# Performance work log

Measured on AMD Instinct MI355X. Metric: run time of the kernel, lower is better.

The kernel has to match this reference:

```python
import jax, jax.numpy as jnp
import numpy as np

MUL = 128            # channel multiplicity (node feature channels)
Z = 10               # number of chemical elements (node_attrs dim)
L_DIMS = (1, 3, 5, 7)   # edge SH irrep dims, lmax=3
MM_DIMS = (1, 3)        # magmom SH irrep dims, lmax=1
AVG_NUM_NEIGHBORS = 20.0
N_NODES = 5000
N_EDGES = 100000
R_DIM = 8            # edge radial feature dim
MM_INV_DIM = 8       # magmom invariant feature dim


def _mlp(x, Ws, act):
    # e3nn FullyConnectedNet: variance-preserving linear layers, act between hidden layers
    for W in Ws[:-1]:
        h = x @ W * (1.0 / np.sqrt(W.shape[0]))
        x = act(h) if act is not None else h
    return x @ Ws[-1] * (1.0 / np.sqrt(Ws[-1].shape[0]))


def _conv_tp(x, sh, w, dims):
    # channelwise 'uvu' tensor product: (MUL x 0e) x SH(l) -> MUL x l per l.
    # x:[E,MUL], sh:[E,sum(dims)], w:[E,MUL,n_l]. CG for 0e x l -> l is trivial.
    outs, off = [], 0
    for l, d in enumerate(dims):
        blk = (w[:, :, l] * x)[:, :, None] * sh[:, None, off:off + d]  # [E,MUL,d]
        outs.append(blk.reshape(x.shape[0], MUL * d))
        off += d
    return jnp.concatenate(outs, axis=-1)


def _per_l_linear(x, Ws, dims):
    # e3nn o3.Linear: per-l channel mixing with 1/sqrt(fan_in) normalization
    outs, off = [], 0
    scale = 1.0 / np.sqrt(MUL)
    for l, d in enumerate(dims):
        blk = x[:, off:off + MUL * d].reshape(-1, MUL, d)
        outs.append((jnp.einsum('nud,uv->nvd', blk, Ws[l]) * scale).reshape(-1, MUL * d))
        off += MUL * d
    return jnp.concatenate(outs, axis=-1)


def _skip_tp(x, attrs, Ws, dims):
    # FullyConnectedTensorProduct(irreps_out, Zx0e, irreps_out): per-l bilinear mix
    outs, off = [], 0
    scale = 1.0 / np.sqrt(MUL * attrs.shape[-1])
    for l, d in enumerate(dims):
        blk = x[:, off:off + MUL * d].reshape(-1, MUL, d)
        outs.append((jnp.einsum('nud,nz,uzv->nvd', blk, attrs, Ws[l]) * scale).reshape(-1, MUL * d))
        off += MUL * d
    return jnp.concatenate(outs, axis=-1)


def _reshape_irreps(x, dims):
    # [N, sum(MUL*d)] -> [N, MUL, sum(d)]
    outs, off = [], 0
    for d in dims:
        outs.append(x[:, off:off + MUL * d].reshape(-1, MUL, d))
        off += MUL * d
    return jnp.concatenate(outs, axis=-1)


def setup_inputs() -> dict:
    key = jax.random.key(0)
    ks = jax.random.split(key, 24)
    E, N = N_EDGES, N_NODES
    inp = {
        'node_attrs': jax.random.uniform(ks[0], (N, Z), jnp.float32),
        'node_feats': jax.random.normal(ks[1], (N, MUL), jnp.float32),
        'edge_attrs': jax.random.normal(ks[2], (E, sum(L_DIMS)), jnp.float32),
        'edge_feats': jax.random.uniform(ks[3], (E, R_DIM), jnp.float32),
        'magmom_node_inv_feats': jax.random.normal(ks[4], (N, MM_INV_DIM), jnp.float32),
        'magmom_node_attrs': jax.random.normal(ks[5], (N, sum(MM_DIMS)), jnp.float32),
        'edge_index': jax.random.randint(ks[6], (2, E), 0, N),
    }
    rin = R_DIM + MM_INV_DIM
    inp['W_up'] = jax.random.normal(ks[7], (MUL, MUL), jnp.float32)
    inp['W_rad1'] = jax.random.normal(ks[8], (rin, 64), jnp.float32)
    inp['W_rad2'] = jax.random.normal(ks[9], (64, 64), jnp.float32)
    inp['W_rad3'] = jax.random.normal(ks[10], (64, 64), jnp.float32)
    inp['W_rad4'] = jax.random.normal(ks[11], (64, MUL * len(L_DIMS)), jnp.float32)  # weight_numel=512
    inp['M_rad1'] = jax.random.normal(ks[12], (rin, 64), jnp.float32)
    inp['M_rad2'] = jax.random.normal(ks[13], (64, 64), jnp.float32)
    inp['M_rad3'] = jax.random.normal(ks[14], (64, 64), jnp.float32)
    inp['M_rad4'] = jax.random.normal(ks[15], (64, MUL * len(MM_DIMS)), jnp.float32)  # weight_numel=256
    inp['W_density'] = jax.random.normal(ks[16], (R_DIM, 1), jnp.float32)
    inp['W_lin'] = jax.random.normal(ks[17], (len(L_DIMS), MUL, MUL), jnp.float32)
    inp['W_mlin'] = jax.random.normal(ks[18], (len(MM_DIMS), MUL, MUL), jnp.float32)
    inp['W_skip'] = jax.random.normal(ks[19], (len(L_DIMS), MUL, Z, MUL), jnp.float32)
    inp['W_mskip'] = jax.random.normal(ks[20], (len(L_DIMS), MUL, Z, MUL), jnp.float32)
    return inp


def reference(node_attrs, node_feats, edge_attrs, edge_feats, magmom_node_inv_feats,
              magmom_node_attrs, W_up, W_rad1, W_rad2, W_rad3, W_rad4,
              M_rad1, M_rad2, M_rad3, M_rad4, W_density, W_lin, W_mlin,
              W_skip, W_mskip, edge_index):
    sender, receiver = edge_index[0], edge_index[1]
    E = edge_attrs.shape[0]
    N = node_feats.shape[0]
    silu = jax.nn.silu

    x = node_feats @ W_up * (1.0 / np.sqrt(MUL))  # linear_up
    xj = x[sender]                                # [E, MUL]
    ef_mm = jnp.concatenate([edge_feats, magmom_node_inv_feats[sender]], axis=-1)  # [E, 16]

    tp_w = _mlp(ef_mm, [W_rad1, W_rad2, W_rad3, W_rad4], silu)          # [E, 512]
    edge_density = jnp.tanh((edge_feats @ W_density * (1.0 / np.sqrt(R_DIM))) ** 2)  # [E, 1]

    w4 = tp_w.reshape(E, MUL, len(L_DIMS))
    pre_mji = _conv_tp(xj, edge_attrs, w4, L_DIMS)                      # [E, 2048]

    w_mm = _mlp(ef_mm, [M_rad1, M_rad2, M_rad3, M_rad4], None).reshape(E, MUL, len(MM_DIMS))
    w_mm = w_mm * pre_mji[:, :MUL][:, :, None]                          # density-gated by scalar part
    magmom_mji = _conv_tp(xj, magmom_node_attrs[sender], w_mm, MM_DIMS) # [E, 512]

    w4b = w4 * magmom_mji[:, :MUL][:, :, None]
    mji = _conv_tp(xj, edge_attrs, w4b, L_DIMS)                         # [E, 2048]

    density = jax.ops.segment_sum(edge_density, receiver, num_segments=N)  # [N, 1]
    msg = jax.ops.segment_sum(mji, receiver, num_segments=N)               # [N, 2048]
    mm_msg = jax.ops.segment_sum(magmom_mji, receiver, num_segments=N)     # [N, 512]

    msg = _per_l_linear(msg, W_lin, L_DIMS) / (density + 1.0)
    msg = _skip_tp(msg, node_attrs, W_skip, L_DIMS)

    mm = _per_l_linear(mm_msg, W_mlin, MM_DIMS) / AVG_NUM_NEIGHBORS
    # magmom_linear maps (128x0e+128x1o) -> target irreps: l=2,3 outputs have no path -> zero
    mm = jnp.concatenate([mm, jnp.zeros((N, MUL * (5 + 7)), mm.dtype)], axis=-1)
    mm = _skip_tp(mm, node_attrs, W_mskip, L_DIMS)

    out1 = _reshape_irreps(msg, L_DIMS)  # [N, 128, 16]
    out2 = _reshape_irreps(mm, L_DIMS)   # [N, 128, 16]
    return jnp.stack([out1, out2], axis=0)
```

## Files before the change

kernel.cpp:

```cpp
#include <hip/hip_runtime.h>
#include <hip/hip_fp16.h>
#include <stdint.h>


__device__ __forceinline__ float silu_f(float x) {
  return x / (1.0f + __expf(-x));
}

union F2H2 { float f; __half2 h; };

__global__ void k_zero_int(int* p, int n) {
  int i = blockIdx.x * blockDim.x + threadIdx.x;
  if (i < n) p[i] = 0;
}

__global__ __launch_bounds__(256) void k_prep(
    const float* __restrict__ M1, const float* __restrict__ M2,
    const float* __restrict__ M3, const float* __restrict__ M4,
    float* __restrict__ Mc) {
  __shared__ float T1[16 * 64];
  __shared__ float T2[16 * 64];
  int t = threadIdx.x;
  for (int i = t; i < 16 * 64; i += 256) {
    int r = i >> 6, c = i & 63;
    float s = 0.f;
    for (int k = 0; k < 64; k++) s += M1[r * 64 + k] * M2[k * 64 + c];
    T1[i] = s;
  }
  __syncthreads();
  for (int i = t; i < 16 * 64; i += 256) {
    int r = i >> 6, c = i & 63;
    float s = 0.f;
    for (int k = 0; k < 64; k++) s += T1[r * 64 + k] * M3[k * 64 + c];
    T2[i] = s;
  }
  __syncthreads();
  for (int i = t; i < 16 * 256; i += 256) {
    int r = i >> 8, c = i & 255;
    float s = 0.f;
    for (int k = 0; k < 64; k++) s += T2[r * 64 + k] * M4[k * 256 + c];
    Mc[i] = s * (1.0f / 2048.0f);
  }
}

__global__ __launch_bounds__(256) void k_w4h(const float* __restrict__ W4,
                                             __half2* __restrict__ W4h) {
  int k = blockIdx.x;
  int t = threadIdx.x;
  W4h[k * 256 + t] =
      __halves2half2(__float2half(W4[k * 512 + t]), __float2half(W4[k * 512 + t + 256]));
}

__global__ __launch_bounds__(128) void k_up(const float* __restrict__ nf,
                                            const float* __restrict__ W,
                                            float* __restrict__ x, int Nn) {
  int n = blockIdx.x;
  int v = threadIdx.x;
  __shared__ float row[128];
  row[v] = nf[n * 128 + v];
  __syncthreads();
  float s = 0.f;
#pragma unroll 8
  for (int k = 0; k < 128; k++) s += row[k] * W[k * 128 + v];
  x[n * 128 + v] = s * 0.08838834764831845f;
}

__global__ void k_count(const int* __restrict__ recv, int* __restrict__ deg, int E) {
  int e = blockIdx.x * blockDim.x + threadIdx.x;
  if (e < E) atomicAdd(&deg[recv[e]], 1);
}

__global__ __launch_bounds__(1024) void k_scan(const int* __restrict__ deg,
                                               int* __restrict__ rowstart,
                                               int* __restrict__ cursor, int Nn) {
  __shared__ int part[1024];
  int t = threadIdx.x;
  int chunk = (Nn + 1023) / 1024;
  int lo = t * chunk;
  int hi = lo + chunk; if (hi > Nn) hi = Nn; if (lo > Nn) lo = Nn;
  int s = 0;
  for (int i = lo; i < hi; i++) s += deg[i];
  part[t] = s;
  __syncthreads();
  for (int o = 1; o < 1024; o <<= 1) {
    int v = (t >= o) ? part[t - o] : 0;
    __syncthreads();
    part[t] += v;
    __syncthreads();
  }
  int base = (t == 0) ? 0 : part[t - 1];
  for (int i = lo; i < hi; i++) {
    rowstart[i] = base;
    cursor[i] = base;
    base += deg[i];
  }
  if (t == 1023) rowstart[Nn] = part[1023];
}

__global__ void k_fill(const int* __restrict__ recv, int* __restrict__ cursor,
                       int* __restrict__ elist, int E) {
  int e = blockIdx.x * blockDim.x + threadIdx.x;
  if (e < E) {
    int p = atomicAdd(&cursor[recv[e]], 1);
    elist[p] = e;
  }
}

__global__ __launch_bounds__(256) void k_edge_hA(
    const float* __restrict__ edge_feats, const float* __restrict__ mminv,
    const int* __restrict__ sender,
    const float* __restrict__ W1, const float* __restrict__ W2,
    const float* __restrict__ W3, const float* __restrict__ Wd,
    float* __restrict__ hAe, float* __restrict__ dens, int E) {
  const int base = blockIdx.x * 8;
  const int t = threadIdx.x;
  __shared__ float ef[8][16];
  __shared__ float hA[8][64];
  __shared__ float hB[8][64];
  const int gwave = t >> 6;
  const int o6 = t & 63;

  if (t < 128) {
    int g = t >> 4, j = t & 15;
    int e = base + g;
    float v = 0.f;
    if (e < E) v = (j < 8) ? edge_feats[e * 8 + j] : mminv[sender[e] * 8 + (j - 8)];
    ef[g][j] = v;
  } else if (t < 136) {
    int g = t - 128;
    int e = base + g;
    if (e < E) {
      float q = 0.f;
#pragma unroll
      for (int k = 0; k < 8; k++) q += edge_feats[e * 8 + k] * Wd[k];
      q *= 0.35355339059327373f;
      dens[e] = tanhf(q * q);
    }
  }
  __syncthreads();

#pragma unroll
  for (int rep = 0; rep < 2; rep++) {
    int g = gwave + rep * 4;
    float s = 0.f;
#pragma unroll
    for (int k = 0; k < 16; k++) s += ef[g][k] * W1[k * 64 + o6];
    hA[g][o6] = silu_f(s * 0.25f);
  }
#pragma unroll
  for (int rep = 0; rep < 2; rep++) {
    int g = gwave + rep * 4;
    float s = 0.f;
#pragma unroll 8
    for (int k = 0; k < 64; k++) s += hA[g][k] * W2[k * 64 + o6];
    hB[g][o6] = silu_f(s * 0.125f);
  }
#pragma unroll
  for (int rep = 0; rep < 2; rep++) {
    int g = gwave + rep * 4;
    float s = 0.f;
#pragma unroll 8
    for (int k = 0; k < 64; k++) s += hB[g][k] * W3[k * 64 + o6];
    int e = base + g;
    if (e < E) hAe[(size_t)e * 64 + o6] = silu_f(s * 0.125f);
  }
}

__global__ __launch_bounds__(256) void k_gather_raw(
    const float* __restrict__ x, const float* __restrict__ edge_attrs,
    const float* __restrict__ edge_feats, const float* __restrict__ mminv,
    const float* __restrict__ mmattrs, const int* __restrict__ sender,
    const __half2* __restrict__ W4h, const float* __restrict__ Mc,
    const float* __restrict__ dens, const float* __restrict__ hAe,
    const int* __restrict__ rowstart, const int* __restrict__ elist,
    float* __restrict__ msg, float* __restrict__ mmr, float* __restrict__ densN,
    int Nn) {
  const int n = blockIdx.x;
  const int t = threadIdx.x;
  const int start = rowstart[n], end = rowstart[n + 1];

  __shared__ float ef[8][16];
  __shared__ float hA[8][64];
  __shared__ float ubuf[8 * 512 + 8 * 256];
  __shared__ float xjs[8][128];
  __shared__ float shs[8][16];
  __shared__ float mmshs[8][4];
  __shared__ float denss[8];
  __shared__ int eS[8], sS[8];

  float (*w4s)[512] = (float (*)[512])ubuf;
  float (*wmms)[256] = (float (*)[256])(ubuf + 8 * 512);

  float accm[8] = {0, 0, 0, 0, 0, 0, 0, 0};
  float accmm0 = 0.f, accmm1 = 0.f;
  float accd = 0.f;

  const int u = t & 127;
  const int half = t >> 7;

  for (int base = start; base < end; base += 8) {
    if (t < 8) {
      int g = t;
      if (base + g < end) {
        int e = elist[base + g];
        eS[g] = e;
        sS[g] = sender[e];
        denss[g] = dens[e];
      } else {
        eS[g] = -1;
        sS[g] = 0;
        denss[g] = 0.f;
      }
    }
    __syncthreads();
    if (t < 128) {
      int g = t >> 4, j = t & 15;
      int e = eS[g];
      shs[g][j] = (e >= 0) ? edge_attrs[e * 16 + j] : 0.f;
      float v = 0.f;
      if (e >= 0) v = (j < 8) ? edge_feats[e * 8 + j] : mminv[sS[g] * 8 + (j - 8)];
      ef[g][j] = v;
    } else if (t < 160) {
      int g = (t - 128) >> 2, j = (t - 128) & 3;
      mmshs[g][j] = (eS[g] >= 0) ? mmattrs[sS[g] * 4 + j] : 0.f;
    }
    for (int i = t; i < 1024; i += 256) {
      int g = i >> 7, uu = i & 127;
      xjs[g][uu] = (eS[g] >= 0) ? x[(size_t)sS[g] * 128 + uu] : 0.f;
    }
    for (int i = t; i < 512; i += 256) {
      int g = i >> 6, k = i & 63;
      hA[g][k] = (eS[g] >= 0) ? hAe[(size_t)eS[g] * 64 + k] : 0.f;
    }
    __syncthreads();

    {
      float a[8] = {0, 0, 0, 0, 0, 0, 0, 0};
      float b[8] = {0, 0, 0, 0, 0, 0, 0, 0};
#pragma unroll 8
      for (int k = 0; k < 64; k++) {
        __half2 w2 = W4h[k * 256 + t];
        float w0 = __low2float(w2);
        float w1 = __high2float(w2);
#pragma unroll
        for (int g = 0; g < 8; g++) {
          float h = hA[g][k];
          a[g] += h * w0;
          b[g] += h * w1;
        }
      }
      int p0 = (t & 3) * 128 + (t >> 2);
      int p1 = (t & 3) * 128 + 64 + (t >> 2);
#pragma unroll
      for (int g = 0; g < 8; g++) {
        w4s[g][p0] = a[g] * 0.125f;
        w4s[g][p1] = b[g] * 0.125f;
      }
    }
    {
      float c[8] = {0, 0, 0, 0, 0, 0, 0, 0};
#pragma unroll
      for (int k = 0; k < 16; k++) {
        float w = Mc[k * 256 + t];
#pragma unroll
        for (int g = 0; g < 8; g++) c[g] += ef[g][k] * w;
      }
      int p = (t & 1) * 128 + (t >> 1);
#pragma unroll
      for (int g = 0; g < 8; g++) wmms[g][p] = c[g];
    }
    __syncthreads();

#pragma unroll 2
    for (int g = 0; g < 8; g++) {
      float w40 = w4s[g][u];
      float w41 = w4s[g][128 + u];
      float w42 = w4s[g][256 + u];
      float w43 = w4s[g][384 + u];
      float wm0 = wmms[g][u];
      float wm1 = wmms[g][128 + u];
      float xj = xjs[g][u];
      float sh0 = shs[g][0];
      float pre0 = w40 * xj * sh0;
      float wg0 = wm0 * pre0;
      float wg1 = wm1 * pre0;
      float mm0 = wg0 * xj * mmshs[g][0];
      float m1 = wg1 * xj;
      float bx = mm0 * xj;
      float b0 = w40 * bx, b1 = w41 * bx, b2 = w42 * bx, b3 = w43 * bx;
      if (half == 0) {
        accmm0 += mm0;
        accmm1 += m1 * mmshs[g][1];
        accm[0] += b0 * sh0;
        accm[1] += b1 * shs[g][1];
        accm[2] += b1 * shs[g][2];
        accm[3] += b1 * shs[g][3];
        accm[4] += b2 * shs[g][4];
        accm[5] += b2 * shs[g][5];
        accm[6] += b2 * shs[g][6];
        accm[7] += b2 * shs[g][7];
      } else {
        accmm0 += m1 * mmshs[g][2];
        accmm1 += m1 * mmshs[g][3];
        accm[0] += b2 * shs[g][8];
        accm[1] += b3 * shs[g][9];
        accm[2] += b3 * shs[g][10];
        accm[3] += b3 * shs[g][11];
        accm[4] += b3 * shs[g][12];
        accm[5] += b3 * shs[g][13];
        accm[6] += b3 * shs[g][14];
        accm[7] += b3 * shs[g][15];
      }
    }
    if (t == 0) {
#pragma unroll
      for (int g = 0; g < 8; g++) accd += denss[g];
    }
  }

  float4* mp = (float4*)(msg + (size_t)n * 2048 + u * 16 + half * 8);
  mp[0] = make_float4(accm[0], accm[1], accm[2], accm[3]);
  mp[1] = make_float4(accm[4], accm[5], accm[6], accm[7]);
  *(float2*)(mmr + (size_t)n * 512 + u * 4 + half * 2) = make_float2(accmm0, accmm1);
  if (t == 0) densN[n] = accd;
}

__global__ void k_zero2(float* __restrict__ out2, int Nn) {
  int i = blockIdx.x * blockDim.x + threadIdx.x;
  if (i < Nn * 128) {
    float4 z = make_float4(0.f, 0.f, 0.f, 0.f);
    float4* p = (float4*)(out2 + (size_t)i * 16);
    p[1] = z;
    p[2] = z;
    p[3] = z;
  }
}

__global__ __launch_bounds__(128) void k_wt(const float* __restrict__ Wskip,
                                            const float* __restrict__ Wmskip,
                                            __half* __restrict__ Wt) {
  int bx = blockIdx.x;
  int L = bx >> 7, u = bx & 127;
  int v = threadIdx.x;
  const float* src = (L < 4) ? (Wskip + (size_t)L * 163840)
                             : (Wmskip + (size_t)(L - 4) * 163840);
  __half* dst = Wt + (((size_t)L * 128 + u) * 128 + v) * 12;
#pragma unroll
  for (int z = 0; z < 10; z++) dst[z] = __float2half(src[u * 1280 + z * 128 + v]);
  dst[10] = __float2half(0.f);
  dst[11] = __float2half(0.f);
}

template <int D, int SP>
__device__ __forceinline__ void skip2_body(
    const float* __restrict__ attrs, const float* __restrict__ in, int in_rs,
    int in_us, int in_cb, const float* __restrict__ Wl,
    const float* __restrict__ densN, float basescl, bool useDinv,
    const __half* __restrict__ Wt, float* __restrict__ outp, int out_cb,
    int Nn, int n0, float* lin_s, float (*attrs_s)[10]) {
  const int t = threadIdx.x;
  for (int i = t; i < 80; i += 256) {
    int nn = i / 10, z = i - nn * 10;
    int n = n0 + nn;
    attrs_s[nn][z] = (n < Nn) ? attrs[n * 10 + z] : 0.f;
  }
  for (int i = t; i < 8 * 128 * D; i += 256) {
    int nn = i / (128 * D);
    int r = i - nn * 128 * D;
    int uu = r / D;
    int m = r - uu * D;
    int n = n0 + nn;
    lin_s[(nn * 128 + uu) * SP + m] =
        (n < Nn) ? in[(size_t)n * in_rs + uu * in_us + in_cb + m] : 0.f;
  }
  __syncthreads();

  const int v = t & 127, hf = t >> 7;

  float lm[4][D];
#pragma unroll
  for (int q = 0; q < 4; q++)
#pragma unroll
    for (int m = 0; m < D; m++) lm[q][m] = 0.f;
  for (int uu = 0; uu < 128; uu++) {
    float wv = Wl[uu * 128 + v];
#pragma unroll
    for (int q = 0; q < 4; q++) {
      const float* ls = &lin_s[((hf * 4 + q) * 128 + uu) * SP];
#pragma unroll
      for (int m = 0; m < D; m++) lm[q][m] += ls[m] * wv;
    }
  }
  __syncthreads();
#pragma unroll
  for (int q = 0; q < 4; q++) {
    int nd = n0 + hf * 4 + q;
    float scl = basescl;
    if (useDinv) scl *= 1.0f / (((nd < Nn) ? densN[nd] : 0.f) + 1.0f);
    float* ls = &lin_s[((hf * 4 + q) * 128 + v) * SP];
#pragma unroll
    for (int m = 0; m < D; m++) ls[m] = lm[q][m] * scl;
  }
  __syncthreads();

  float ar[4][10];
#pragma unroll
  for (int q = 0; q < 4; q++)
#pragma unroll
    for (int z = 0; z < 10; z++) ar[q][z] = attrs_s[hf * 4 + q][z];

  float acc[4][D];
#pragma unroll
  for (int q = 0; q < 4; q++)
#pragma unroll
    for (int m = 0; m < D; m++) acc[q][m] = 0.f;

  const __half* wp0 = Wt + (size_t)v * 12;
  for (int u = 0; u < 128; u++) {
    const __half* wp = wp0 + (size_t)u * 1536;
    const float2* fp = (const float2*)wp;
    float2 q0 = fp[0];
    float2 q1 = fp[1];
    float2 q2 = fp[2];
    F2H2 c0, c1, c2, c3, c4;
    c0.f = q0.x; c1.f = q0.y; c2.f = q1.x; c3.f = q1.y; c4.f = q2.x;
    float wr[10];
    wr[0] = __low2float(c0.h); wr[1] = __high2float(c0.h);
    wr[2] = __low2float(c1.h); wr[3] = __high2float(c1.h);
    wr[4] = __low2float(c2.h); wr[5] = __high2float(c2.h);
    wr[6] = __low2float(c3.h); wr[7] = __high2float(c3.h);
    wr[8] = __low2float(c4.h); wr[9] = __high2float(c4.h);
#pragma unroll
    for (int q = 0; q < 4; q++) {
      float wn = 0.f;
#pragma unroll
      for (int z = 0; z < 10; z++) wn += ar[q][z] * wr[z];
      const float* ls = &lin_s[((hf * 4 + q) * 128 + u) * SP];
#pragma unroll
      for (int m = 0; m < D; m++) acc[q][m] += ls[m] * wn;
    }
  }
#pragma unroll
  for (int q = 0; q < 4; q++) {
    int n = n0 + hf * 4 + q;
    if (n < Nn) {
      float* op = outp + (size_t)n * 2048 + v * 16 + out_cb;
#pragma unroll
      for (int m = 0; m < D; m++) op[m] = acc[q][m] * 0.027950849718747371f;
    }
  }
}

__global__ __launch_bounds__(256) void k_skip2(
    const float* __restrict__ attrs, const float* __restrict__ msg,
    const float* __restrict__ mmr, const float* __restrict__ densN,
    const float* __restrict__ Wlin, const float* __restrict__ Wmlin,
    const __half* __restrict__ Wt, float* __restrict__ out, int Nn) {
  __shared__ float lin_s[8 * 128 * 8];
  __shared__ float attrs_s[8][10];
  const int n0 = blockIdx.x * 8;
  const int job = blockIdx.y;
  const __half* Wtj = Wt + (size_t)job * 128 * 128 * 12;
  const float scl = 0.08838834764831845f;
  const float sm = 0.08838834764831845f / 20.0f;
  switch (job) {
    case 0: skip2_body<1, 1>(attrs, msg, 2048, 16, 0, Wlin, densN, scl, true, Wtj, out, 0, Nn, n0, lin_s, attrs_s); break;
    case 1: skip2_body<3, 4>(attrs, msg, 2048, 16, 1, Wlin + 16384, densN, scl, true, Wtj, out, 1, Nn, n0, lin_s, attrs_s); break;
    case 2: skip2_body<5, 8>(attrs, msg, 2048, 16, 4, Wlin + 32768, densN, scl, true, Wtj, out, 4, Nn, n0, lin_s, attrs_s); break;
    case 3: skip2_body<7, 8>(attrs, msg, 2048, 16, 9, Wlin + 49152, densN, scl, true, Wtj, out, 9, Nn, n0, lin_s, attrs_s); break;
    case 4: skip2_body<1, 1>(attrs, mmr, 512, 4, 0, Wmlin, densN, sm, false, Wtj, out + (size_t)Nn * 2048, 0, Nn, n0, lin_s, attrs_s); break;
    case 5: skip2_body<3, 4>(attrs, mmr, 512, 4, 1, Wmlin + 16384, densN, sm, false, Wtj, out + (size_t)Nn * 2048, 1, Nn, n0, lin_s, attrs_s); break;
  }
}

__global__ __launch_bounds__(256) void k_gather_f(
    const float* __restrict__ x, const float* __restrict__ edge_attrs,
    const float* __restrict__ edge_feats, const float* __restrict__ mminv,
    const float* __restrict__ mmattrs, const int* __restrict__ sender,
    const float* __restrict__ W1, const float* __restrict__ W2,
    const float* __restrict__ W3, const float* __restrict__ W4,
    const float* __restrict__ Mc, const float* __restrict__ Wd,
    const float* __restrict__ Wlin, const float* __restrict__ Wmlin,
    const int* __restrict__ rowstart, const int* __restrict__ elist,
    float* __restrict__ linm, float* __restrict__ linmm, int Nn) {
  const int n = blockIdx.x;
  const int t = threadIdx.x;
  const int start = rowstart[n], end = rowstart[n + 1];

  __shared__ float ef[8][16];
  __shared__ float hA[8][64];
  __shared__ float hB[8][64];
  __shared__ float ubuf[8 * 512 + 8 * 256];
  __shared__ float xjs[8][128];
  __shared__ float shs[8][16];
  __shared__ float mmshs[8][4];
  __shared__ float denss[8];
  __shared__ int eS[8], sS[8];
  __shared__ float dsum_s;

  float (*w4s)[512] = (float (*)[512])ubuf;
  float (*wmms)[256] = (float (*)[256])(ubuf + 8 * 512);
  float (*msg_s)[17] = (float (*)[17])ubuf;
  float (*mm_s)[5] = (float (*)[5])(ubuf + 128 * 17);

  float accm[8] = {0, 0, 0, 0, 0, 0, 0, 0};
  float accmm0 = 0.f, accmm1 = 0.f;
  float accd = 0.f;

  const int u = t & 127;
  const int half = t >> 7;
  const int gwave = t >> 6;
  const int o6 = t & 63;

  for (int base = start; base < end; base += 8) {
    if (t < 8) {
      int g = t;
      if (base + g < end) {
        int e = elist[base + g];
        eS[g] = e;
        sS[g] = sender[e];
      } else {
        eS[g] = -1;
        sS[g] = 0;
        denss[g] = 0.f;
      }
    }
    __syncthreads();
    if (t < 128) {
      int g = t >> 4, j = t & 15;
      int e = eS[g];
      shs[g][j] = (e >= 0) ? edge_attrs[e * 16 + j] : 0.f;
      float v = 0.f;
      if (e >= 0) v = (j < 8) ? edge_feats[e * 8 + j] : mminv[sS[g] * 8 + (j - 8)];
      ef[g][j] = v;
    } else if (t < 160) {
      int g = (t - 128) >> 2, j = (t - 128) & 3;
      mmshs[g][j] = (eS[g] >= 0) ? mmattrs[sS[g] * 4 + j] : 0.f;
    }
    for (int i = t; i < 1024; i += 256) {
      int g = i >> 7, uu = i & 127;
      xjs[g][uu] = (eS[g] >= 0) ? x[(size_t)sS[g] * 128 + uu] : 0.f;
    }
    if (t < 8 && eS[t] >= 0) {
      int e = eS[t];
      float q = 0.f;
#pragma unroll
      for (int k = 0; k < 8; k++) q += edge_feats[e * 8 + k] * Wd[k];
      q *= 0.35355339059327373f;
      denss[t] = tanhf(q * q);
    }
    __syncthreads();

#pragma unroll
    for (int rep = 0; rep < 2; rep++) {
      int g = gwave + rep * 4;
      float s = 0.f;
#pragma unroll
      for (int k = 0; k < 16; k++) s += ef[g][k] * W1[k * 64 + o6];
      hA[g][o6] = silu_f(s * 0.25f);
    }
#pragma unroll
    for (int rep = 0; rep < 2; rep++) {
      int g = gwave + rep * 4;
      float s = 0.f;
#pragma unroll 8
      for (int k = 0; k < 64; k++) s += hA[g][k] * W2[k * 64 + o6];
      hB[g][o6] = silu_f(s * 0.125f);
    }
#pragma unroll
    for (int rep = 0; rep < 2; rep++) {
      int g = gwave + rep * 4;
      float s = 0.f;
#pragma unroll 8
      for (int k = 0; k < 64; k++) s += hB[g][k] * W3[k * 64 + o6];
      hA[g][o6] = silu_f(s * 0.125f);
    }
    __syncthreads();
    {
      float a[8] = {0, 0, 0, 0, 0, 0, 0, 0};
      float b[8] = {0, 0, 0, 0, 0, 0, 0, 0};
#pragma unroll 8
      for (int k = 0; k < 64; k++) {
        float w0 = W4[k * 512 + t];
        float w1 = W4[k * 512 + t + 256];
#pragma unroll
        for (int g = 0; g < 8; g++) {
          float h = hA[g][k];
          a[g] += h * w0;
          b[g] += h * w1;
        }
      }
      int p0 = (t & 3) * 128 + (t >> 2);
      int p1 = (t & 3) * 128 + 64 + (t >> 2);
#pragma unroll
      for (int g = 0; g < 8; g++) {
        w4s[g][p0] = a[g] * 0.125f;
        w4s[g][p1] = b[g] * 0.125f;
      }
    }
    {
      float c[8] = {0, 0, 0, 0, 0, 0, 0, 0};
#pragma unroll
      for (int k = 0; k < 16; k++) {
        float w = Mc[k * 256 + t];
#pragma unroll
        for (int g = 0; g < 8; g++) c[g] += ef[g][k] * w;
      }
      int p = (t & 1) * 128 + (t >> 1);
#pragma unroll
      for (int g = 0; g < 8; g++) wmms[g][p] = c[g];
    }
    __syncthreads();
#pragma unroll 2
    for (int g = 0; g < 8; g++) {
      float xj = xjs[g][u];
      float sh0 = shs[g][0];
      float w40 = w4s[g][u];
      float w41 = w4s[g][128 + u];
      float w42 = w4s[g][256 + u];
      float w43 = w4s[g][384 + u];
      float pre0 = w40 * xj * sh0;
      float wg0 = wmms[g][u] * pre0;
      float wg1 = wmms[g][128 + u] * pre0;
      float mm0 = wg0 * xj * mmshs[g][0];
      float m1 = wg1 * xj;
      float bx = mm0 * xj;
      float b0 = w40 * bx, b1 = w41 * bx, b2 = w42 * bx, b3 = w43 * bx;
      if (half == 0) {
        accmm0 += mm0;
        accmm1 += m1 * mmshs[g][1];
        accm[0] += b0 * sh0;
        accm[1] += b1 * shs[g][1];
        accm[2] += b1 * shs[g][2];
        accm[3] += b1 * shs[g][3];
        accm[4] += b2 * shs[g][4];
        accm[5] += b2 * shs[g][5];
        accm[6] += b2 * shs[g][6];
        accm[7] += b2 * shs[g][7];
      } else {
        accmm0 += m1 * mmshs[g][2];
        accmm1 += m1 * mmshs[g][3];
        accm[0] += b2 * shs[g][8];
        accm[1] += b3 * shs[g][9];
        accm[2] += b3 * shs[g][10];
        accm[3] += b3 * shs[g][11];
        accm[4] += b3 * shs[g][12];
        accm[5] += b3 * shs[g][13];
        accm[6] += b3 * shs[g][14];
        accm[7] += b3 * shs[g][15];
      }
    }
    if (t == 0) {
#pragma unroll
      for (int g = 0; g < 8; g++) accd += denss[g];
    }
  }

  __syncthreads();
#pragma unroll
  for (int j = 0; j < 8; j++) msg_s[u][half * 8 + j] = accm[j];
  mm_s[u][half * 2 + 0] = accmm0;
  mm_s[u][half * 2 + 1] = accmm1;
  if (t == 0) dsum_s = accd;
  __syncthreads();
  const float dinv = 1.0f / (dsum_s + 1.0f);

  float outl[8] = {0, 0, 0, 0, 0, 0, 0, 0};
  if (half == 0) {
    for (int uu = 0; uu < 128; uu++) {
      float wl0 = Wlin[uu * 128 + u];
      float wl1 = Wlin[16384 + uu * 128 + u];
      float wl2 = Wlin[32768 + uu * 128 + u];
      outl[0] += msg_s[uu][0] * wl0;
      outl[1] += msg_s[uu][1] * wl1;
      outl[2] += msg_s[uu][2] * wl1;
      outl[3] += msg_s[uu][3] * wl1;
      outl[4] += msg_s[uu][4] * wl2;
      outl[5] += msg_s[uu][5] * wl2;
      outl[6] += msg_s[uu][6] * wl2;
      outl[7] += msg_s[uu][7] * wl2;
    }
  } else {
    for (int uu = 0; uu < 128; uu++) {
      float wl2 = Wlin[32768 + uu * 128 + u];
      float wl3 = Wlin[49152 + uu * 128 + u];
      outl[0] += msg_s[uu][8] * wl2;
      outl[1] += msg_s[uu][9] * wl3;
      outl[2] += msg_s[uu][10] * wl3;
      outl[3] += msg_s[uu][11] * wl3;
      outl[4] += msg_s[uu][12] * wl3;
      outl[5] += msg_s[uu][13] * wl3;
      outl[6] += msg_s[uu][14] * wl3;
      outl[7] += msg_s[uu][15] * wl3;
    }
  }
  const float sclv = 0.08838834764831845f * dinv;
  float4 v0 = make_float4(outl[0] * sclv, outl[1] * sclv, outl[2] * sclv, outl[3] * sclv);
  float4 v1 = make_float4(outl[4] * sclv, outl[5] * sclv, outl[6] * sclv, outl[7] * sclv);
  float4* lp = (float4*)(linm + (size_t)n * 2048 + u * 16 + half * 8);
  lp[0] = v0;
  lp[1] = v1;

  float om0 = 0.f, om1 = 0.f;
  if (half == 0) {
    for (int uu = 0; uu < 128; uu++) {
      om0 += mm_s[uu][0] * Wmlin[uu * 128 + u];
      om1 += mm_s[uu][1] * Wmlin[16384 + uu * 128 + u];
    }
  } else {
    for (int uu = 0; uu < 128; uu++) {
      float wm1 = Wmlin[16384 + uu * 128 + u];
      om0 += mm_s[uu][2] * wm1;
      om1 += mm_s[uu][3] * wm1;
    }
  }
  const float sm = 0.08838834764831845f / 20.0f;
  *(float2*)(linmm + (size_t)n * 512 + u * 4 + half * 2) = make_float2(om0 * sm, om1 * sm);
}

template <int D, int SP>
__device__ __forceinline__ void skip_body2(
    const float* __restrict__ attrs, const float* __restrict__ in, int in_rs,
    int in_us, int in_cb, const __half* __restrict__ Wt, float* __restrict__ outp,
    int out_cb, int Nn, int n0, float* lin_s, float (*attrs_s)[10]) {
  const int t = threadIdx.x;
  for (int i = t; i < 160; i += 256) {
    int nn = i / 10, z = i - nn * 10;
    int n = n0 + nn;
    attrs_s[nn][z] = (n < Nn) ? attrs[n * 10 + z] : 0.f;
  }
  for (int i = t; i < 16 * 128 * D; i += 256) {
    int nn = i / (128 * D);
    int r = i - nn * 128 * D;
    int uu = r / D;
    int m = r - uu * D;
    int n = n0 + nn;
    lin_s[(nn * 128 + uu) * SP + m] =
        (n < Nn) ? in[(size_t)n * in_rs + uu * in_us + in_cb + m] : 0.f;
  }
  __syncthreads();

  const int v = t & 127, hf = t >> 7;
  float ar[8][10];
#pragma unroll
  for (int q = 0; q < 8; q++)
#pragma unroll
    for (int z = 0; z < 10; z++) ar[q][z] = attrs_s[hf * 8 + q][z];

  float acc[8][D];
#pragma unroll
  for (int q = 0; q < 8; q++)
#pragma unroll
    for (int m = 0; m < D; m++) acc[q][m] = 0.f;

  const __half* wp0 = Wt + (size_t)v * 12;
  for (int u = 0; u < 128; u++) {
    const __half* wp = wp0 + (size_t)u * 1536;
    const float2* fp = (const float2*)wp;
    float2 q0 = fp[0];
    float2 q1 = fp[1];
    float2 q2 = fp[2];
    F2H2 c0, c1, c2, c3, c4;
    c0.f = q0.x; c1.f = q0.y; c2.f = q1.x; c3.f = q1.y; c4.f = q2.x;
    float wr[10];
    wr[0] = __low2float(c0.h); wr[1] = __high2float(c0.h);
    wr[2] = __low2float(c1.h); wr[3] = __high2float(c1.h);
    wr[4] = __low2float(c2.h); wr[5] = __high2float(c2.h);
    wr[6] = __low2float(c3.h); wr[7] = __high2float(c3.h);
    wr[8] = __low2float(c4.h); wr[9] = __high2float(c4.h);
#pragma unroll
    for (int q = 0; q < 8; q++) {
      float wn = 0.f;
#pragma unroll
      for (int z = 0; z < 10; z++) wn += ar[q][z] * wr[z];
      const float* ls = &lin_s[((hf * 8 + q) * 128 + u) * SP];
#pragma unroll
      for (int m = 0; m < D; m++) acc[q][m] += ls[m] * wn;
    }
  }
#pragma unroll
  for (int q = 0; q < 8; q++) {
    int n = n0 + hf * 8 + q;
    if (n < Nn) {
      float* op = outp + (size_t)n * 2048 + v * 16 + out_cb;
#pragma unroll
      for (int m = 0; m < D; m++) op[m] = acc[q][m] * 0.027950849718747371f;
    }
  }
}

__global__ __launch_bounds__(256) void k_skip(
    const float* __restrict__ attrs, const float* __restrict__ linm,
    const float* __restrict__ linmm, const __half* __restrict__ Wt,
    float* __restrict__ out, int Nn) {
  __shared__ float lin_s[16 * 128 * 8];
  __shared__ float attrs_s[16][10];
  const int n0 = blockIdx.x * 16;
  const int job = blockIdx.y;
  const __half* Wtj = Wt + (size_t)job * 128 * 128 * 12;
  switch (job) {
    case 0: skip_body2<1, 1>(attrs, linm, 2048, 16, 0, Wtj, out, 0, Nn, n0, lin_s, attrs_s); break;
    case 1: skip_body2<3, 4>(attrs, linm, 2048, 16, 1, Wtj, out, 1, Nn, n0, lin_s, attrs_s); break;
    case 2: skip_body2<5, 8>(attrs, linm, 2048, 16, 4, Wtj, out, 4, Nn, n0, lin_s, attrs_s); break;
    case 3: skip_body2<7, 8>(attrs, linm, 2048, 16, 9, Wtj, out, 9, Nn, n0, lin_s, attrs_s); break;
    case 4: skip_body2<1, 1>(attrs, linmm, 512, 4, 0, Wtj, out + (size_t)Nn * 2048, 0, Nn, n0, lin_s, attrs_s); break;
    case 5: skip_body2<3, 4>(attrs, linmm, 512, 4, 1, Wtj, out + (size_t)Nn * 2048, 1, Nn, n0, lin_s, attrs_s); break;
  }
}

extern "C" void kernel_launch(void* const* d_in, const int* in_sizes, int n_in,
                              void* d_out, int out_size, void* d_ws, size_t ws_size,
                              hipStream_t stream) {
  const float* node_attrs = (const float*)d_in[0];
  const float* node_feats = (const float*)d_in[1];
  const float* edge_attrs = (const float*)d_in[2];
  const float* edge_feats = (const float*)d_in[3];
  const float* mminv = (const float*)d_in[4];
  const float* mmattrs = (const float*)d_in[5];
  const int* edge_index = (const int*)d_in[6];
  const float* W_up = (const float*)d_in[7];
  const float* W1 = (const float*)d_in[8];
  const float* W2 = (const float*)d_in[9];
  const float* W3 = (const float*)d_in[10];
  const float* W4 = (const float*)d_in[11];
  const float* M1 = (const float*)d_in[12];
  const float* M2 = (const float*)d_in[13];
  const float* M3 = (const float*)d_in[14];
  const float* M4 = (const float*)d_in[15];
  const float* Wd = (const float*)d_in[16];
  const float* Wlin = (const float*)d_in[17];
  const float* Wmlin = (const float*)d_in[18];
  const float* Wskip = (const float*)d_in[19];
  const float* Wmskip = (const float*)d_in[20];

  const int N = in_sizes[1] / 128;
  const int E = in_sizes[2] / 16;
  const int* sender = edge_index;
  const int* recv = edge_index + E;

  float* ws = (float*)d_ws;
  float* x = ws;     ws += (size_t)N * 128;
  float* Mc = ws;    ws += 16 * 256;
  __half* Wt = (__half*)ws;  ws += (size_t)6 * 128 * 128 * 12 / 2;
  __half2* W4h = (__half2*)ws; ws += 64 * 256;
  float* msg = ws;   ws += (size_t)N * 2048;
  float* mmr = ws;   ws += (size_t)N * 512;
  float* densN = ws; ws += N;
  float* dens = ws;  ws += E;
  int* ibuf = (int*)ws;
  int* rowstart = ibuf;
  int* deg = ibuf + (N + 1);
  int* cursor = deg + N;
  int* elist = cursor + N;
  float* hAe = (float*)(((uintptr_t)(elist + E) + 63) & ~(uintptr_t)63);
  size_t need = (size_t)((char*)hAe - (char*)d_ws) + (size_t)E * 64 * 4 + 256;
  const bool mainPath = ws_size >= need;

  k_zero_int<<<(N + 255) / 256, 256, 0, stream>>>(deg, N);
  k_prep<<<1, 256, 0, stream>>>(M1, M2, M3, M4, Mc);
  k_wt<<<768, 128, 0, stream>>>(Wskip, Wmskip, Wt);
  k_w4h<<<64, 256, 0, stream>>>(W4, W4h);
  k_up<<<N, 128, 0, stream>>>(node_feats, W_up, x, N);
  k_count<<<(E + 255) / 256, 256, 0, stream>>>(recv, deg, E);
  k_scan<<<1, 1024, 0, stream>>>(deg, rowstart, cursor, N);
  k_fill<<<(E + 255) / 256, 256, 0, stream>>>(recv, cursor, elist, E);

  if (mainPath) {
    k_edge_hA<<<(E + 7) / 8, 256, 0, stream>>>(edge_feats, mminv, sender, W1,
                                               W2, W3, Wd, hAe, dens, E);
    k_gather_raw<<<N, 256, 0, stream>>>(x, edge_attrs, edge_feats, mminv,
                                        mmattrs, sender, W4h, Mc, dens, hAe,
                                        rowstart, elist, msg, mmr, densN, N);
    k_zero2<<<(N * 128 + 255) / 256, 256, 0, stream>>>((float*)d_out + (size_t)N * 2048, N);
    dim3 gs2((N + 7) / 8, 6);
    k_skip2<<<gs2, 256, 0, stream>>>(node_attrs, msg, mmr, densN, Wlin, Wmlin,
                                     Wt, (float*)d_out, N);
  } else {
    k_gather_f<<<N, 256, 0, stream>>>(x, edge_attrs, edge_feats, mminv,
                                      mmattrs, sender, W1, W2, W3, W4, Mc, Wd,
                                      Wlin, Wmlin, rowstart, elist, msg, mmr, N);
    k_zero2<<<(N * 128 + 255) / 256, 256, 0, stream>>>((float*)d_out + (size_t)N * 2048, N);
    dim3 gs((N + 15) / 16, 6);
    k_skip<<<gs, 256, 0, stream>>>(node_attrs, msg, mmr, Wt, (float*)d_out, N);
  }
}
```

Before: 896.2 us.

## Precompute per-edge W4 radial weights in fp16 before node gather

Adds a new path where a per-edge kernel runs the radial MLP through the final W4 layer and stores the 512 per-edge weights as fp16. The node-level gather then reads these precomputed weights instead of redoing the 64x512 W4 projection from hidden activations inside the gather. This takes the large matmul out of the irregular gather loop, at the cost of a bigger workspace (E*1KB) and more memory traffic, plus fp16 rounding of the weights. The old hidden-activation path is kept as a fallback when the workspace is too small.

```diff
diff --git a/kernel.cpp b/kernel.cpp
--- a/kernel.cpp
+++ b/kernel.cpp
@@ -104,6 +104,237 @@
     int p = atomicAdd(&cursor[recv[e]], 1);
     elist[p] = e;
   }
+}
+
+__global__ __launch_bounds__(256) void k_edge_w4(
+    const float* __restrict__ edge_feats, const float* __restrict__ mminv,
+    const int* __restrict__ sender,
+    const float* __restrict__ W1, const float* __restrict__ W2,
+    const float* __restrict__ W3, const float* __restrict__ W4,
+    const float* __restrict__ Wd, __half* __restrict__ w4e,
+    float* __restrict__ dens, int E) {
+  const int base = blockIdx.x * 8;
+  const int t = threadIdx.x;
+  __shared__ float ef[8][16];
+  __shared__ float hA[8][64];
+  __shared__ float hB[8][64];
+  __shared__ float w4s[8][512];
+  const int gwave = t >> 6;
+  const int o6 = t & 63;
+
+  if (t < 128) {
+    int g = t >> 4, j = t & 15;
+    int e = base + g;
+    float v = 0.f;
+    if (e < E) v = (j < 8) ? edge_feats[e * 8 + j] : mminv[sender[e] * 8 + (j - 8)];
+    ef[g][j] = v;
+  } else if (t < 136) {
+    int g = t - 128;
+    int e = base + g;
+    if (e < E) {
+      float q = 0.f;
+#pragma unroll
+      for (int k = 0; k < 8; k++) q += edge_feats[e * 8 + k] * Wd[k];
+      q *= 0.35355339059327373f;
+      dens[e] = tanhf(q * q);
+    }
+  }
+  __syncthreads();
+
+#pragma unroll
+  for (int rep = 0; rep < 2; rep++) {
+    int g = gwave + rep * 4;
+    float s = 0.f;
+#pragma unroll
+    for (int k = 0; k < 16; k++) s += ef[g][k] * W1[k * 64 + o6];
+    hA[g][o6] = silu_f(s * 0.25f);
+  }
+#pragma unroll
+  for (int rep = 0; rep < 2; rep++) {
+    int g = gwave + rep * 4;
+    float s = 0.f;
+#pragma unroll 8
+    for (int k = 0; k < 64; k++) s += hA[g][k] * W2[k * 64 + o6];
+    hB[g][o6] = silu_f(s * 0.125f);
+  }
+#pragma unroll
+  for (int rep = 0; rep < 2; rep++) {
+    int g = gwave + rep * 4;
+    float s = 0.f;
+#pragma unroll 8
+    for (int k = 0; k < 64; k++) s += hB[g][k] * W3[k * 64 + o6];
+    hA[g][o6] = silu_f(s * 0.125f);
+  }
+  __syncthreads();
+
+  {
+    float a[8] = {0, 0, 0, 0, 0, 0, 0, 0};
+    float b[8] = {0, 0, 0, 0, 0, 0, 0, 0};
+#pragma unroll 8
+    for (int k = 0; k < 64; k++) {
+      float w0 = W4[k * 512 + t];
+      float w1 = W4[k * 512 + t + 256];
+#pragma unroll
+      for (int g = 0; g < 8; g++) {
+        float h = hA[g][k];
+        a[g] += h * w0;
+        b[g] += h * w1;
+      }
+    }
+    int p0 = (t & 3) * 128 + (t >> 2);
+    int p1 = (t & 3) * 128 + 64 + (t >> 2);
+#pragma unroll
+    for (int g = 0; g < 8; g++) {
+      w4s[g][p0] = a[g] * 0.125f;
+      w4s[g][p1] = b[g] * 0.125f;
+    }
+  }
+  __syncthreads();
+
+  __half2* dst = (__half2*)w4e;
+#pragma unroll
+  for (int g = 0; g < 8; g++) {
+    int e = base + g;
+    if (e < E) {
+      dst[(size_t)e * 256 + t] =
+          __halves2half2(__float2half(w4s[g][2 * t]), __float2half(w4s[g][2 * t + 1]));
+    }
+  }
+}
+
+__global__ __launch_bounds__(256) void k_gather_c(
+    const float* __restrict__ x, const float* __restrict__ edge_attrs,
+    const float* __restrict__ edge_feats, const float* __restrict__ mminv,
+    const float* __restrict__ mmattrs, const int* __restrict__ sender,
+    const float* __restrict__ Mc, const __half* __restrict__ w4e,
+    const float* __restrict__ dens,
+    const int* __restrict__ rowstart, const int* __restrict__ elist,
+    float* __restrict__ msg, float* __restrict__ mmr, float* __restrict__ densN,
+    int Nn) {
+  const int n = blockIdx.x;
+  const int t = threadIdx.x;
+  const int start = rowstart[n], end = rowstart[n + 1];
+
+  __shared__ float ef[8][16];
+  __shared__ float wmms[8][256];
+  __shared__ float xjs[8][128];
+  __shared__ float shs[8][16];
+  __shared__ float mmshs[8][4];
+  __shared__ float denss[8];
+  __shared__ int eS[8], sS[8];
+
+  float accm[8] = {0, 0, 0, 0, 0, 0, 0, 0};
+  float accmm0 = 0.f, accmm1 = 0.f;
+  float accd = 0.f;
+
+  const int u = t & 127;
+  const int half = t >> 7;
+
+  for (int base = start; base < end; base += 8) {
+    if (t < 8) {
+      int g = t;
+      if (base + g < end) {
+        int e = elist[base + g];
+        eS[g] = e;
+        sS[g] = sender[e];
+        denss[g] = dens[e];
+      } else {
+        eS[g] = -1;
+        sS[g] = 0;
+        denss[g] = 0.f;
+      }
+    }
+    __syncthreads();
+    int erA[8];
+#pragma unroll
+    for (int g = 0; g < 8; g++) {
+      int ev = eS[g];
+      erA[g] = ev < 0 ? 0 : ev;
+    }
+    if (t < 128) {
+      int g = t >> 4, j = t & 15;
+      int e = eS[g];
+      shs[g][j] = (e >= 0) ? edge_attrs[e * 16 + j] : 0.f;
+      float v = 0.f;
+      if (e >= 0) v = (j < 8) ? edge_feats[e * 8 + j] : mminv[sS[g] * 8 + (j - 8)];
+      ef[g][j] = v;
+    } else if (t < 160) {
+      int g = (t - 128) >> 2, j = (t - 128) & 3;
+      mmshs[g][j] = (eS[g] >= 0) ? mmattrs[sS[g] * 4 + j] : 0.f;
+    }
+    for (int i = t; i < 1024; i += 256) {
+      int g = i >> 7, uu = i & 127;
+      xjs[g][uu] = (eS[g] >= 0) ? x[(size_t)sS[g] * 128 + uu] : 0.f;
+    }
+    __syncthreads();
+
+    {
+      float c[8] = {0, 0, 0, 0, 0, 0, 0, 0};
+#pragma unroll
+      for (int k = 0; k < 16; k++) {
+        float w = Mc[k * 256 + t];
+#pragma unroll
+        for (int g = 0; g < 8; g++) c[g] += ef[g][k] * w;
+      }
+      int p = (t & 1) * 128 + (t >> 1);
+#pragma unroll
+      for (int g = 0; g < 8; g++) wmms[g][p] = c[g];
+    }
+    __syncthreads();
+
+#pragma unroll 2
+    for (int g = 0; g < 8; g++) {
+      const __half* w4g = w4e + (size_t)erA[g] * 512;
+      float w40 = __half2float(w4g[u]);
+      float w41 = __half2float(w4g[128 + u]);
+      float w42 = __half2float(w4g[256 + u]);
+      float w43 = __half2float(w4g[384 + u]);
+      float wm0 = wmms[g][u];
+      float wm1 = wmms[g][128 + u];
+      float xj = xjs[g][u];
+      float sh0 = shs[g][0];
+      float pre0 = w40 * xj * sh0;
+      float wg0 = wm0 * pre0;
+      float wg1 = wm1 * pre0;
+      float mm0 = wg0 * xj * mmshs[g][0];
+      float m1 = wg1 * xj;
+      float bx = mm0 * xj;
+      float b0 = w40 * bx, b1 = w41 * bx, b2 = w42 * bx, b3 = w43 * bx;
+      if (half == 0) {
+        accmm0 += mm0;
+        accmm1 += m1 * mmshs[g][1];
+        accm[0] += b0 * sh0;
+        accm[1] += b1 * shs[g][1];
+        accm[2] += b1 * shs[g][2];
+        accm[3] += b1 * shs[g][3];
+        accm[4] += b2 * shs[g][4];
+        accm[5] += b2 * shs[g][5];
+        accm[6] += b2 * shs[g][6];
+        accm[7] += b2 * shs[g][7];
+      } else {
+        accmm0 += m1 * mmshs[g][2];
+        accmm1 += m1 * mmshs[g][3];
+        accm[0] += b2 * shs[g][8];
+        accm[1] += b3 * shs[g][9];
+        accm[2] += b3 * shs[g][10];
+        accm[3] += b3 * shs[g][11];
+        accm[4] += b3 * shs[g][12];
+        accm[5] += b3 * shs[g][13];
+        accm[6] += b3 * shs[g][14];
+        accm[7] += b3 * shs[g][15];
+      }
+    }
+    if (t == 0) {
+#pragma unroll
+      for (int g = 0; g < 8; g++) accd += denss[g];
+    }
+  }
+
+  float4* mp = (float4*)(msg + (size_t)n * 2048 + u * 16 + half * 8);
+  mp[0] = make_float4(accm[0], accm[1], accm[2], accm[3]);
+  mp[1] = make_float4(accm[4], accm[5], accm[6], accm[7]);
+  *(float2*)(mmr + (size_t)n * 512 + u * 4 + half * 2) = make_float2(accmm0, accmm1);
+  if (t == 0) densN[n] = accd;
 }
 
 __global__ __launch_bounds__(256) void k_edge_hA(
@@ -852,20 +1083,34 @@
   int* deg = ibuf + (N + 1);
   int* cursor = deg + N;
   int* elist = cursor + N;
-  float* hAe = (float*)(((uintptr_t)(elist + E) + 63) & ~(uintptr_t)63);
-  size_t need = (size_t)((char*)hAe - (char*)d_ws) + (size_t)E * 64 * 4 + 256;
-  const bool mainPath = ws_size >= need;
+  char* tail = (char*)(((uintptr_t)(elist + E) + 63) & ~(uintptr_t)63);
+  size_t tailOff = (size_t)(tail - (char*)d_ws);
+  size_t needA = tailOff + (size_t)E * 512 * 2 + 256;
+  size_t needB = tailOff + (size_t)E * 64 * 4 + 256;
+  __half* w4e = (__half*)tail;
+  float* hAe = (float*)tail;
+  const int mode = (ws_size >= needA) ? 0 : (ws_size >= needB ? 1 : 2);
 
   k_zero_int<<<(N + 255) / 256, 256, 0, stream>>>(deg, N);
   k_prep<<<1, 256, 0, stream>>>(M1, M2, M3, M4, Mc);
   k_wt<<<768, 128, 0, stream>>>(Wskip, Wmskip, Wt);
-  k_w4h<<<64, 256, 0, stream>>>(W4, W4h);
   k_up<<<N, 128, 0, stream>>>(node_feats, W_up, x, N);
   k_count<<<(E + 255) / 256, 256, 0, stream>>>(recv, deg, E);
   k_scan<<<1, 1024, 0, stream>>>(deg, rowstart, cursor, N);
   k_fill<<<(E + 255) / 256, 256, 0, stream>>>(recv, cursor, elist, E);
 
-  if (mainPath) {
+  if (mode == 0) {
+    k_edge_w4<<<(E + 7) / 8, 256, 0, stream>>>(edge_feats, mminv, sender, W1,
+                                               W2, W3, W4, Wd, w4e, dens, E);
+    k_gather_c<<<N, 256, 0, stream>>>(x, edge_attrs, edge_feats, mminv,
+                                      mmattrs, sender, Mc, w4e, dens, rowstart,
+                                      elist, msg, mmr, densN, N);
+    k_zero2<<<(N * 128 + 255) / 256, 256, 0, stream>>>((float*)d_out + (size_t)N * 2048, N);
+    dim3 gs2((N + 7) / 8, 6);
+    k_skip2<<<gs2, 256, 0, stream>>>(node_attrs, msg, mmr, densN, Wlin, Wmlin,
+                                     Wt, (float*)d_out, N);
+  } else if (mode == 1) {
+    k_w4h<<<64, 256, 0, stream>>>(W4, W4h);
     k_edge_hA<<<(E + 7) / 8, 256, 0, stream>>>(edge_feats, mminv, sender, W1,
                                                W2, W3, Wd, hAe, dens, E);
     k_gather_raw<<<N, 256, 0, stream>>>(x, edge_attrs, edge_feats, mminv,
```

Measured after the change: 818.6 us. -8.7%, faster.
